# Kernel optimization log

Hardware: AMD Instinct MI355X
Metric: run time of the kernel (lower is better)

Reference implementation:

```python
import jax, jax.numpy as jnp
import numpy as np

N_NODES = 50000
N_EDGES = 800000
IN_DIM = 128
EDGE_DIM = 16
N_HEADS = 8
OUT_DIM = 16  # per head


def setup_inputs() -> dict:
    key = jax.random.key(0)
    ks = jax.random.split(key, 6)
    x = jax.random.normal(ks[0], (N_NODES, IN_DIM), dtype=jnp.float32)
    edge_attr = jax.random.normal(ks[1], (N_EDGES, EDGE_DIM), dtype=jnp.float32)
    W_node = jax.random.normal(ks[2], (N_HEADS, IN_DIM, OUT_DIM), dtype=jnp.float32) * 0.1
    W_edge = jax.random.normal(ks[3], (N_HEADS, EDGE_DIM, OUT_DIM), dtype=jnp.float32) * 0.1
    src = jax.random.randint(ks[4], (N_EDGES,), 0, N_NODES, dtype=jnp.int32)
    dst = jax.random.randint(ks[5], (N_EDGES,), 0, N_NODES, dtype=jnp.int32)
    return {"x": x, "edge_attr": edge_attr, "W_node": W_node, "W_edge": W_edge,
            "src": src, "dst": dst}


def reference(x, edge_attr, W_node, W_edge, src, dst):
    # Multi-head edge-gated GAT layer (EG_GATLayer), use_edge=use_gate=True.
    H, _, D = W_node.shape
    N = x.shape[0]
    scale = 1.0 / jnp.sqrt(jnp.asarray(D, x.dtype))

    h = jnp.einsum('ni,hid->nhd', x, W_node)          # [N,H,D] per-head node proj
    e = jnp.einsum('ei,hid->ehd', edge_attr, W_edge)  # [E,H,D] per-head edge proj

    q = h[dst]                                        # [E,H,D] gather dst nodes
    k = h[src]                                        # [E,H,D] gather src nodes

    # edge-conditioned attention logits, LeakyReLU as in GAT
    logits = ((q * k).sum(-1) + e.sum(-1)) * scale    # [E,H]
    logits = jax.nn.leaky_relu(logits, 0.2)

    # segment softmax over each destination node's incoming edges
    m = jax.ops.segment_max(logits, dst, num_segments=N)  # [N,H]
    m = jnp.where(jnp.isfinite(m), m, 0.0)
    m = jax.lax.stop_gradient(m)
    ex = jnp.exp(logits - m[dst])                     # [E,H]
    denom = jax.ops.segment_sum(ex, dst, num_segments=N)  # [N,H]
    alpha = ex / (denom[dst] + 1e-9)                  # [E,H]

    # edge-gated messages, scatter-aggregate to dst
    msg = k * jax.nn.sigmoid(e) * alpha[..., None]    # [E,H,D]
    out = jax.ops.segment_sum(msg, dst, num_segments=N)   # [N,H,D]
    return out.reshape(N, H * D)                      # concat heads
```

## Files before the change

kernel.cpp:

```cpp
#include <hip/hip_runtime.h>
#include <math.h>


#define LOG2E 1.44269504088896340736f
#define C_QK  0.36067376022224085f

typedef _Float16 h2 __attribute__((ext_vector_type(2)));
typedef _Float16 h4 __attribute__((ext_vector_type(4)));
typedef _Float16 h8 __attribute__((ext_vector_type(8)));
typedef float    f4 __attribute__((ext_vector_type(4)));

__device__ __forceinline__ float fdot2(h2 a, h2 b, float c) {
    return __builtin_amdgcn_fdot2(a, b, c, false);
}
__device__ __forceinline__ h2 bch(unsigned u) {
    return __builtin_bit_cast(h2, u);
}
__device__ __forceinline__ unsigned pkh2(float a, float b) {
    h2 p = { (_Float16)a, (_Float16)b };
    return __builtin_bit_cast(unsigned, p);
}

#define DPP_ADD(x, ctrl)                                                       \
    x += __builtin_bit_cast(float, __builtin_amdgcn_update_dpp(                \
             0, __builtin_bit_cast(int, x), (ctrl), 0xF, 0xF, false))

__global__ __launch_bounds__(256) void k_gp(
    const float* __restrict__ x, const float* __restrict__ Wn,
    const float* __restrict__ ea, const float* __restrict__ We,
    const int* __restrict__ src, const int* __restrict__ dst,
    _Float16* __restrict__ h16, _Float16* __restrict__ ea16,
    int2* __restrict__ csrbin, int* __restrict__ counts,
    unsigned* __restrict__ gatetab, int N, int E, int nGemmB)
{
    int t = threadIdx.x;

    if ((int)blockIdx.x < nGemmB) {
        int lane = t & 63, wid = t >> 6;
        int rt = blockIdx.x * 4 + wid;
        if (rt * 16 >= N) return;
        int r = lane & 15, kb = lane >> 4;

        const float* xrow = x + (size_t)(rt * 16 + r) * 128 + kb * 8;
        h8 A[4];
#pragma unroll
        for (int kk = 0; kk < 4; ++kk) {
            f4 a0 = *(const f4*)(xrow + kk * 32);
            f4 a1 = *(const f4*)(xrow + kk * 32 + 4);
            A[kk] = h8{(_Float16)a0.x,(_Float16)a0.y,(_Float16)a0.z,(_Float16)a0.w,
                       (_Float16)a1.x,(_Float16)a1.y,(_Float16)a1.z,(_Float16)a1.w};
        }
        for (int h = 0; h < 8; ++h) {
            const float* wb = Wn + h * 2048 + (kb * 8) * 16 + r;
            f4 acc = {0.f, 0.f, 0.f, 0.f};
#pragma unroll
            for (int kk = 0; kk < 4; ++kk) {
                const float* wk = wb + (size_t)kk * 32 * 16;
                h8 B;
#pragma unroll
                for (int i = 0; i < 8; ++i) B[i] = (_Float16)wk[i * 16];
                acc = __builtin_amdgcn_mfma_f32_16x16x32_f16(A[kk], B, acc, 0, 0, 0);
            }
#pragma unroll
            for (int j = 0; j < 4; ++j) {
                h16[(size_t)(rt * 16 + 4 * kb + j) * 128 + h * 16 + r] =
                    (_Float16)acc[j];
            }
        }
        return;
    }

    int e = ((int)blockIdx.x - nGemmB) * 256 + t;
    if (e < E) {
        int dn = dst[e];
        int r = atomicAdd(counts + dn, 1);
        csrbin[((size_t)dn << 6) + r] = make_int2(e << 5, src[e] << 8);
        const float4* ap = (const float4*)(ea + (size_t)e * 16);
        float4 a0 = ap[0], a1 = ap[1], a2 = ap[2], a3 = ap[3];
        h4* op = (h4*)(ea16 + ((size_t)e << 4));
        op[0] = h4{(_Float16)a0.x, (_Float16)a0.y, (_Float16)a0.z, (_Float16)a0.w};
        op[1] = h4{(_Float16)a1.x, (_Float16)a1.y, (_Float16)a1.z, (_Float16)a1.w};
        op[2] = h4{(_Float16)a2.x, (_Float16)a2.y, (_Float16)a2.z, (_Float16)a2.w};
        op[3] = h4{(_Float16)a3.x, (_Float16)a3.y, (_Float16)a3.z, (_Float16)a3.w};
    }

    if (blockIdx.x == gridDim.x - 1 && t < 64) {
        int lane = t;
        int head = lane >> 3, dd = lane & 7, d0 = dd * 2;
        const float* Wh = We + head * 256;
        unsigned* row = gatetab + lane * 20;
#pragma unroll
        for (int i = 0; i < 8; ++i) {
            row[i]     = pkh2(Wh[(2*i)*16 + d0]     * -LOG2E,
                              Wh[(2*i+1)*16 + d0]   * -LOG2E);
            row[8 + i] = pkh2(Wh[(2*i)*16 + d0 + 1] * -LOG2E,
                              Wh[(2*i+1)*16 + d0+1] * -LOG2E);
        }
        float cs0 = 0.f, cs1 = 0.f;
#pragma unroll
        for (int k = 0; k < 16; ++k) {
            cs0 += Wh[d0 * 16 + k];
            cs1 += Wh[(d0 + 1) * 16 + k];
        }
        row[16] = pkh2(cs0 * C_QK, cs1 * C_QK);
    }
}

__global__ __launch_bounds__(256) void k_alloc(
    const int* __restrict__ counts, int2* __restrict__ seg,
    int* __restrict__ gcur, int N)
{
    int i = blockIdx.x * 256 + threadIdx.x;
    int lane = threadIdx.x & 63;
    int v = (i < N) ? counts[i] : 0;
    int incl = v;
#pragma unroll
    for (int o = 1; o < 64; o <<= 1) {
        int u = __shfl_up(incl, o);
        if (lane >= o) incl += u;
    }
    int total = __shfl(incl, 63);
    int base = 0;
    if (lane == 63) base = atomicAdd(gcur, total);
    base = __shfl(base, 63);
    int st = base + incl - v;
    if (i < N) seg[i] = make_int2(st, v);
}

__global__ __launch_bounds__(256) void k_compact(
    const int2* __restrict__ csrbin, const int2* __restrict__ seg,
    int2* __restrict__ csr, int N)
{
    int t = threadIdx.x;
    int lane = t & 63, wid = t >> 6;
    int n = blockIdx.x * 4 + wid;
    if (n >= N) return;
    int2 sg = seg[n];
    if (lane < sg.y)
        csr[sg.x + lane] = csrbin[((size_t)n << 6) + lane];
}

__global__ __launch_bounds__(64) void k_fused12(
    const _Float16* __restrict__ h16, const _Float16* __restrict__ ea16,
    const int2* __restrict__ csr, const unsigned* __restrict__ gatetab,
    const int2* __restrict__ seg, float* __restrict__ out, int N)
{
    int lane = threadIdx.x;
    int n = blockIdx.x;
    int dd = lane & 7;

    const uint4* tb = (const uint4*)(gatetab + lane * 20);
    uint4 t0 = tb[0], t1 = tb[1], t2 = tb[2], t3 = tb[3];
    h2 cs2 = bch(gatetab[lane * 20 + 16]);
    h2 wa[8], wb[8];
    wa[0]=bch(t0.x); wa[1]=bch(t0.y); wa[2]=bch(t0.z); wa[3]=bch(t0.w);
    wa[4]=bch(t1.x); wa[5]=bch(t1.y); wa[6]=bch(t1.z); wa[7]=bch(t1.w);
    wb[0]=bch(t2.x); wb[1]=bch(t2.y); wb[2]=bch(t2.z); wb[3]=bch(t2.w);
    wb[4]=bch(t3.x); wb[5]=bch(t3.y); wb[6]=bch(t3.z); wb[7]=bch(t3.w);

    const char* hb = (const char*)h16;
    const char* eb = (const char*)ea16;
    unsigned l4 = (unsigned)lane << 2;
    unsigned dd4 = (unsigned)dd << 2;

    h2 q2 = *(const h2*)(hb + ((size_t)n << 8) + l4);
    q2 = q2 * h2{ (_Float16)C_QK, (_Float16)C_QK };
    int2 sg = seg[n];
    int s0  = __builtin_amdgcn_readfirstlane(sg.x);
    int deg = __builtin_amdgcn_readfirstlane(sg.y);

    float acc0 = 0.f, acc1 = 0.f, den = 0.f;
#pragma unroll 8
    for (int j = 0; j < deg; ++j) {
        int2 ce = csr[s0 + j];
        unsigned eoff = (unsigned)ce.x;
        h2 kv2 = *(const h2*)(hb + (unsigned)ce.y + l4);
        uint4 r0 = *(const uint4*)(eb + eoff);
        uint4 r1 = *(const uint4*)(eb + eoff + 16);
        h2 ea2 = *(const h2*)(eb + eoff + dd4);

        float part = fdot2(q2, kv2, 0.f);
        part = fdot2(ea2, cs2, part);
        DPP_ADD(part, 0xB1);
        DPP_ADD(part, 0x4E);
        DPP_ADD(part, 0x141);

        float lg = fmaxf(part, 0.2f * part);
        float pa = exp2f(lg);

        float ev0 = 0.f, ev1 = 0.f;
        ev0 = fdot2(bch(r0.x), wa[0], ev0);  ev1 = fdot2(bch(r0.x), wb[0], ev1);
        ev0 = fdot2(bch(r0.y), wa[1], ev0);  ev1 = fdot2(bch(r0.y), wb[1], ev1);
        ev0 = fdot2(bch(r0.z), wa[2], ev0);  ev1 = fdot2(bch(r0.z), wb[2], ev1);
        ev0 = fdot2(bch(r0.w), wa[3], ev0);  ev1 = fdot2(bch(r0.w), wb[3], ev1);
        ev0 = fdot2(bch(r1.x), wa[4], ev0);  ev1 = fdot2(bch(r1.x), wb[4], ev1);
        ev0 = fdot2(bch(r1.y), wa[5], ev0);  ev1 = fdot2(bch(r1.y), wb[5], ev1);
        ev0 = fdot2(bch(r1.z), wa[6], ev0);  ev1 = fdot2(bch(r1.z), wb[6], ev1);
        ev0 = fdot2(bch(r1.w), wa[7], ev0);  ev1 = fdot2(bch(r1.w), wb[7], ev1);
        float sg0 = __builtin_amdgcn_rcpf(1.f + exp2f(ev0));
        float sg1 = __builtin_amdgcn_rcpf(1.f + exp2f(ev1));

        den += pa;
        acc0 = fmaf(pa * sg0, (float)kv2.x, acc0);
        acc1 = fmaf(pa * sg1, (float)kv2.y, acc1);
    }
    float idn = __builtin_amdgcn_rcpf(den + 1e-9f);
    *(float2*)(out + ((size_t)n << 7) + (lane << 1)) =
        make_float2(acc0 * idn, acc1 * idn);
}

extern "C" void kernel_launch(void* const* d_in, const int* in_sizes, int n_in,
                              void* d_out, int out_size, void* d_ws, size_t ws_size,
                              hipStream_t stream)
{
    const float* x  = (const float*)d_in[0];
    const float* ea = (const float*)d_in[1];
    const float* Wn = (const float*)d_in[2];
    const float* We = (const float*)d_in[3];
    const int*  src = (const int*)d_in[4];
    const int*  dst = (const int*)d_in[5];
    float* out = (float*)d_out;

    int N = in_sizes[0] / 128;
    int E = in_sizes[4];

    char* ws = (char*)d_ws;
    int2*      csrbin = (int2*)ws;
    int2*      csr    = (int2*)(ws + (size_t)N * 512);
    _Float16*  ea16   = (_Float16*)(ws + (size_t)N * 512 + (size_t)E * 8);
    _Float16*  h16    = ea16 + (size_t)E * 16;
    int2*      seg    = (int2*)(h16 + (size_t)N * 128);
    int*       counts = (int*)(seg + N);
    int*       gcur   = counts + N;
    unsigned*  gatetab= (unsigned*)(gcur + 1);

    hipMemsetAsync(counts, 0, (size_t)(N + 1) * sizeof(int), stream);

    int nGemmB = ((N + 15) / 16 + 3) / 4;
    int nEdgeB = (E + 255) / 256;
    k_gp     <<<nGemmB + nEdgeB, 256, 0, stream>>>(x, Wn, ea, We, src, dst,
                                                   h16, ea16, csrbin, counts,
                                                   gatetab, N, E, nGemmB);
    k_alloc  <<<(N + 255) / 256, 256, 0, stream>>>(counts, seg, gcur, N);
    k_compact<<<(N + 3) / 4,     256, 0, stream>>>(csrbin, seg, csr, N);
    k_fused12<<<N,               64, 0, stream>>>(h16, ea16, csr, gatetab,
                                                  seg, out, N);
}
```

Baseline: 174.8 us.

## Read fixed-stride edge bins directly and drop scan and compaction kernels

Removes the prefix-scan allocation kernel and the CSR compaction kernel. The fused attention kernel now reads each node's fixed 64-slot bin from csrbin with one coalesced per-lane load and broadcasts the entries with shuffles. This saves two launches plus a full read and write pass over the edge list. It assumes node in-degree never exceeds 64, and each iteration now carries two cross-lane shuffles.

```diff
diff --git a/kernel.cpp b/kernel.cpp
--- a/kernel.cpp
+++ b/kernel.cpp
@@ -106,44 +106,10 @@
     }
 }
 
-__global__ __launch_bounds__(256) void k_alloc(
-    const int* __restrict__ counts, int2* __restrict__ seg,
-    int* __restrict__ gcur, int N)
-{
-    int i = blockIdx.x * 256 + threadIdx.x;
-    int lane = threadIdx.x & 63;
-    int v = (i < N) ? counts[i] : 0;
-    int incl = v;
-#pragma unroll
-    for (int o = 1; o < 64; o <<= 1) {
-        int u = __shfl_up(incl, o);
-        if (lane >= o) incl += u;
-    }
-    int total = __shfl(incl, 63);
-    int base = 0;
-    if (lane == 63) base = atomicAdd(gcur, total);
-    base = __shfl(base, 63);
-    int st = base + incl - v;
-    if (i < N) seg[i] = make_int2(st, v);
-}
-
-__global__ __launch_bounds__(256) void k_compact(
-    const int2* __restrict__ csrbin, const int2* __restrict__ seg,
-    int2* __restrict__ csr, int N)
-{
-    int t = threadIdx.x;
-    int lane = t & 63, wid = t >> 6;
-    int n = blockIdx.x * 4 + wid;
-    if (n >= N) return;
-    int2 sg = seg[n];
-    if (lane < sg.y)
-        csr[sg.x + lane] = csrbin[((size_t)n << 6) + lane];
-}
-
-__global__ __launch_bounds__(64) void k_fused12(
+__global__ __launch_bounds__(64) void k_fused14(
     const _Float16* __restrict__ h16, const _Float16* __restrict__ ea16,
-    const int2* __restrict__ csr, const unsigned* __restrict__ gatetab,
-    const int2* __restrict__ seg, float* __restrict__ out, int N)
+    const int2* __restrict__ csrbin, const unsigned* __restrict__ gatetab,
+    const int* __restrict__ counts, float* __restrict__ out, int N)
 {
     int lane = threadIdx.x;
     int n = blockIdx.x;
@@ -165,16 +131,17 @@
 
     h2 q2 = *(const h2*)(hb + ((size_t)n << 8) + l4);
     q2 = q2 * h2{ (_Float16)C_QK, (_Float16)C_QK };
-    int2 sg = seg[n];
-    int s0  = __builtin_amdgcn_readfirstlane(sg.x);
-    int deg = __builtin_amdgcn_readfirstlane(sg.y);
+    int deg = __builtin_amdgcn_readfirstlane(counts[n]);
+
+    int2 ceL = csrbin[((size_t)n << 6) + lane];
+    int ceX = ceL.x, ceY = ceL.y;
 
     float acc0 = 0.f, acc1 = 0.f, den = 0.f;
 #pragma unroll 8
     for (int j = 0; j < deg; ++j) {
-        int2 ce = csr[s0 + j];
-        unsigned eoff = (unsigned)ce.x;
-        h2 kv2 = *(const h2*)(hb + (unsigned)ce.y + l4);
+        unsigned eoff = (unsigned)__shfl(ceX, j);
+        unsigned koff = (unsigned)__shfl(ceY, j);
+        h2 kv2 = *(const h2*)(hb + koff + l4);
         uint4 r0 = *(const uint4*)(eb + eoff);
         uint4 r1 = *(const uint4*)(eb + eoff + 16);
         h2 ea2 = *(const h2*)(eb + eoff + dd4);
@@ -226,23 +193,18 @@
 
     char* ws = (char*)d_ws;
     int2*      csrbin = (int2*)ws;
-    int2*      csr    = (int2*)(ws + (size_t)N * 512);
-    _Float16*  ea16   = (_Float16*)(ws + (size_t)N * 512 + (size_t)E * 8);
+    _Float16*  ea16   = (_Float16*)(ws + (size_t)N * 512);
     _Float16*  h16    = ea16 + (size_t)E * 16;
-    int2*      seg    = (int2*)(h16 + (size_t)N * 128);
-    int*       counts = (int*)(seg + N);
-    int*       gcur   = counts + N;
-    unsigned*  gatetab= (unsigned*)(gcur + 1);
-
-    hipMemsetAsync(counts, 0, (size_t)(N + 1) * sizeof(int), stream);
+    int*       counts = (int*)(h16 + (size_t)N * 128);
+    unsigned*  gatetab= (unsigned*)(counts + N);
+
+    hipMemsetAsync(counts, 0, (size_t)N * sizeof(int), stream);
 
     int nGemmB = ((N + 15) / 16 + 3) / 4;
     int nEdgeB = (E + 255) / 256;
     k_gp     <<<nGemmB + nEdgeB, 256, 0, stream>>>(x, Wn, ea, We, src, dst,
                                                    h16, ea16, csrbin, counts,
                                                    gatetab, N, E, nGemmB);
-    k_alloc  <<<(N + 255) / 256, 256, 0, stream>>>(counts, seg, gcur, N);
-    k_compact<<<(N + 3) / 4,     256, 0, stream>>>(csrbin, seg, csr, N);
-    k_fused12<<<N,               64, 0, stream>>>(h16, ea16, csr, gatetab,
-                                                  seg, out, N);
-}
+    k_fused14<<<N,               64, 0, stream>>>(h16, ea16, csrbin, gatetab,
+                                                  counts, out, N);
+}
```

New measurement: 156.5 us (median of 2 runs). 1.12x faster.
